# Optimization experiments

Measured on AMD Instinct MI355X. Metric: run time of the kernel, lower is better.

The kernel has to match this reference:

```python
import jax, jax.numpy as jnp
import numpy as np

SLEN, BSZ = 256, 8
NUM_HEAD, DIM_HEAD = 16, 64
IN_DIM = NUM_HEAD * DIM_HEAD  # 1024
LN_EPS = 1e-5


def setup_inputs() -> dict:
    key = jax.random.key(0)
    ks = jax.random.split(key, 6)
    std = 1.0 / np.sqrt(DIM_HEAD)
    std_q = 0.01 / np.sqrt(DIM_HEAD)
    beta_init = -1.0
    h = jax.random.normal(ks[0], (SLEN, BSZ, IN_DIM), dtype=jnp.float32)
    W_y = std * jax.random.normal(ks[1], (1, NUM_HEAD, DIM_HEAD, DIM_HEAD), dtype=jnp.float32)
    W_q = std_q * jax.random.normal(ks[2], (1, NUM_HEAD, DIM_HEAD, DIM_HEAD), dtype=jnp.float32)
    W_k = std * jax.random.normal(ks[3], (1, NUM_HEAD, DIM_HEAD, DIM_HEAD), dtype=jnp.float32)
    w_b = beta_init + std * jax.random.normal(ks[4], (1, NUM_HEAD, DIM_HEAD, 4), dtype=jnp.float32)
    out_w = std * jax.random.normal(ks[5], (IN_DIM, NUM_HEAD * DIM_HEAD), dtype=jnp.float32)
    ln_gamma = jnp.ones((IN_DIM,), dtype=jnp.float32)
    ln_beta = jnp.zeros((IN_DIM,), dtype=jnp.float32)
    return {"h": h, "W_y": W_y, "W_q": W_q, "W_k": W_k, "w_b": w_b,
            "out_w": out_w, "ln_gamma": ln_gamma, "ln_beta": ln_beta}


def _srwm_scan(x, W_y, W_q, W_k, w_b):
    # x: (slen, B, H, d); fast weights broadcast over batch
    bsz = x.shape[1]
    Wy0 = jnp.broadcast_to(W_y, (bsz,) + W_y.shape[1:])
    Wq0 = jnp.broadcast_to(W_q, (bsz,) + W_q.shape[1:])
    Wk0 = jnp.broadcast_to(W_k, (bsz,) + W_k.shape[1:])
    wb0 = jnp.broadcast_to(w_b, (bsz,) + w_b.shape[1:])

    def step(carry, x_t):
        Wy, Wq, Wk, wb = carry
        # generate outputs with W_{t-1}
        y = jnp.einsum('bhij,bhj->bhi', Wy, x_t)
        q = jax.nn.softmax(jnp.einsum('bhij,bhj->bhi', Wq, x_t), axis=-1)
        k = jax.nn.softmax(jnp.einsum('bhij,bhj->bhi', Wk, x_t), axis=-1)
        beta = jax.nn.sigmoid(jnp.einsum('bhjc,bhj->bhc', wb, x_t))  # (B,H,4)
        qmk = q - k
        def upd(W, b):
            dv = jnp.einsum('bhij,bhj->bhi', W, qmk)  # W q - W k
            return W + b[..., None, None] * dv[..., :, None] * k[..., None, :]
        Wy_n = upd(Wy, beta[..., 0])
        Wq_n = upd(Wq, beta[..., 1])
        Wk_n = upd(Wk, beta[..., 2])
        dvb = jnp.einsum('bhjc,bhj->bhc', wb, qmk)  # (B,H,4)
        wb_n = wb + beta[..., 3][..., None, None] * k[..., :, None] * dvb[..., None, :]
        return (Wy_n, Wq_n, Wk_n, wb_n), y

    _, ys = jax.lax.scan(step, (Wy0, Wq0, Wk0, wb0), x)
    return ys  # (slen, B, H, d)


def reference(h, W_y, W_q, W_k, w_b, out_w, ln_gamma, ln_beta):
    slen, bsz, _ = h.shape
    x = h.reshape(slen, bsz, NUM_HEAD, DIM_HEAD)
    ys = _srwm_scan(x, W_y, W_q, W_k, w_b)
    out = ys.reshape(slen, bsz, NUM_HEAD * DIM_HEAD)
    out = out @ out_w.T  # (slen, bsz, in_dim), no bias
    # dropout p=0 (eval): identity
    mu = jnp.mean(h, axis=-1, keepdims=True)
    var = jnp.mean(jnp.square(h - mu), axis=-1, keepdims=True)
    h_ln = (h - mu) * jax.lax.rsqrt(var + LN_EPS) * ln_gamma + ln_beta
    return h_ln + out
```

## Files before the change

### kernel.cpp

```cpp
#include <hip/hip_runtime.h>
#include <hip/hip_bf16.h>

#define SLEN  256
#define BSZ   8
#define NHEAD 16
#define DHEAD 64
#define INDIM 1024
#define LN_EPS 1e-5f

typedef __attribute__((ext_vector_type(4))) float f32x4;
typedef __attribute__((ext_vector_type(8))) short bf16x8;

__device__ __forceinline__ int f_as_i(float f) { union { float f; int i; } u; u.f = f; return u.i; }
__device__ __forceinline__ float i_as_f(int i) { union { float f; int i; } u; u.i = i; return u.f; }

__device__ inline unsigned short f2bf(float x) {
  __hip_bfloat16 b = __float2bfloat16(x);
  union { __hip_bfloat16 b; unsigned short u; } cv;
  cv.b = b;
  return cv.u;
}

template <int CTRL>
__device__ __forceinline__ float dpp0(float x) {
  return i_as_f(__builtin_amdgcn_update_dpp(0, f_as_i(x), CTRL, 0xF, 0xF, true));
}

__device__ __forceinline__ float pair_other(float x) { return dpp0<0xB1>(x); }

__device__ __forceinline__ float wave_sum64(float v) {
  v += dpp0<0x111>(v);
  v += dpp0<0x112>(v);
  v += dpp0<0x114>(v);
  v += dpp0<0x118>(v);
  v += dpp0<0x142>(v);
  v += dpp0<0x143>(v);
  return i_as_f(__builtin_amdgcn_readlane(f_as_i(v), 63));
}

__global__ __launch_bounds__(512, 1) void scan_prep_k(
    const float* __restrict__ h,
    const float* __restrict__ Wy0,
    const float* __restrict__ Wq0,
    const float* __restrict__ Wk0,
    const float* __restrict__ wb0,
    const float* __restrict__ outw,
    unsigned short* __restrict__ outw_bf,
    float* __restrict__ stats,
    unsigned short* __restrict__ ys_bf) {
  const int bid = blockIdx.x;
  const int tid = threadIdx.x;

  if (bid >= 128) {
    const int pb = bid - 128;
    if (pb < 512) {
      int i = (pb * 512 + tid) * 4;
      float4 v = *(const float4*)(outw + i);
      ushort4 o;
      o.x = f2bf(v.x); o.y = f2bf(v.y); o.z = f2bf(v.z); o.w = f2bf(v.w);
      *(ushort4*)(outw_bf + i) = o;
    } else {
      int r = pb - 512;
      const float* row = h + (size_t)r * INDIM;
      float2 v = *(const float2*)(row + tid * 2);
      float s  = v.x + v.y;
      float s2 = v.x * v.x + v.y * v.y;
      s  = wave_sum64(s);
      s2 = wave_sum64(s2);
      __shared__ float ls[8], ls2[8];
      int wvv = tid >> 6;
      if ((tid & 63) == 0) { ls[wvv] = s; ls2[wvv] = s2; }
      __syncthreads();
      if (tid == 0) {
        float S = 0.f, S2 = 0.f;
        #pragma unroll
        for (int i = 0; i < 8; ++i) { S += ls[i]; S2 += ls2[i]; }
        float mu = S * (1.0f / INDIM);
        float var = S2 * (1.0f / INDIM) - mu * mu;
        stats[2 * r]     = mu;
        stats[2 * r + 1] = rsqrtf(var + LN_EPS);
      }
    }
    return;
  }

  const int chain = bid;
  const int b    = chain >> 4;
  const int head = chain & 15;
  const int wv   = __builtin_amdgcn_readfirstlane(tid >> 6);
  const int lane = tid & 63;

  __shared__ __align__(16) float xbuf[2][64];
  __shared__ __align__(16) float eqk[2][2][64];
  __shared__ __align__(16) float ssub[2][4];
  __shared__ __align__(16) float betabuf[2][4];

  const float* xrow0 = h + (size_t)b * INDIM + head * DHEAD;

  if (wv < 6) {
    const int m    = wv >> 1;
    const int half = wv & 1;
    const int r    = half * 32 + (lane >> 1);
    const int j0   = (lane & 1) * 32;
    const float* Wsel = (m == 0) ? Wy0 : ((m == 1) ? Wq0 : Wk0);
    const float* wrow = Wsel + (size_t)head * DHEAD * DHEAD + (size_t)r * DHEAD + j0;
    float w[32];
    #pragma unroll
    for (int g = 0; g < 8; ++g) {
      float4 t4 = *(const float4*)(wrow + g * 4);
      w[g * 4] = t4.x; w[g * 4 + 1] = t4.y; w[g * 4 + 2] = t4.z; w[g * 4 + 3] = t4.w;
    }
    __syncthreads();

    for (int t = 0; t < SLEN; ++t) {
      const int buf = t & 1;
      float a0 = 0.f, a1 = 0.f, a2 = 0.f, a3 = 0.f;
      #pragma unroll
      for (int g = 0; g < 8; ++g) {
        float4 x4 = *(const float4*)(&xbuf[buf][j0 + g * 4]);
        a0 += w[g * 4]     * x4.x;
        a1 += w[g * 4 + 1] * x4.y;
        a2 += w[g * 4 + 2] * x4.z;
        a3 += w[g * 4 + 3] * x4.w;
      }
      float v = (a0 + a1) + (a2 + a3);
      v += pair_other(v);

      if (m == 0) {
        if (!(lane & 1))
          ys_bf[(size_t)(t * BSZ + b) * INDIM + head * DHEAD + r] = f2bf(v);
      } else {
        float e = __expf(v);
        if (!(lane & 1)) eqk[buf][m - 1][r] = e;
        float sh = wave_sum64(e) * 0.5f;
        if (lane == 0) ssub[buf][(m - 1) * 2 + half] = sh;
      }
      __syncthreads();

      float4 ss = *(const float4*)(&ssub[buf][0]);
      float rq = __fdividef(1.f, ss.x + ss.y);
      float rk = __fdividef(1.f, ss.z + ss.w);
      float bet = betabuf[buf][m];
      float ek[32];
      float dq0 = 0.f, dq1 = 0.f, dq2 = 0.f, dq3 = 0.f;
      float dk0 = 0.f, dk1 = 0.f, dk2 = 0.f, dk3 = 0.f;
      #pragma unroll
      for (int g = 0; g < 8; ++g) {
        float4 q4 = *(const float4*)(&eqk[buf][0][j0 + g * 4]);
        float4 k4 = *(const float4*)(&eqk[buf][1][j0 + g * 4]);
        ek[g * 4] = k4.x; ek[g * 4 + 1] = k4.y; ek[g * 4 + 2] = k4.z; ek[g * 4 + 3] = k4.w;
        dq0 += w[g * 4]     * q4.x;
        dq1 += w[g * 4 + 1] * q4.y;
        dq2 += w[g * 4 + 2] * q4.z;
        dq3 += w[g * 4 + 3] * q4.w;
        dk0 += w[g * 4]     * k4.x;
        dk1 += w[g * 4 + 1] * k4.y;
        dk2 += w[g * 4 + 2] * k4.z;
        dk3 += w[g * 4 + 3] * k4.w;
      }
      float dv = rq * ((dq0 + dq1) + (dq2 + dq3)) - rk * ((dk0 + dk1) + (dk2 + dk3));
      dv += pair_other(dv);
      float c = bet * dv * rk;
      #pragma unroll
      for (int g = 0; g < 8; ++g) {
        w[g * 4]     += c * ek[g * 4];
        w[g * 4 + 1] += c * ek[g * 4 + 1];
        w[g * 4 + 2] += c * ek[g * 4 + 2];
        w[g * 4 + 3] += c * ek[g * 4 + 3];
      }
    }
  } else if (wv == 6) {
    const float* wbrow = wb0 + (size_t)head * DHEAD * 4 + lane * 4;
    float4 wbv = *(const float4*)wbrow;
    __syncthreads();

    for (int t = 0; t < SLEN; ++t) {
      const int buf = t & 1;
      float xv = xbuf[buf][lane];
      float p0 = wave_sum64(wbv.x * xv);
      float p1 = wave_sum64(wbv.y * xv);
      float p2 = wave_sum64(wbv.z * xv);
      float p3 = wave_sum64(wbv.w * xv);
      float b0 = __fdividef(1.f, 1.f + __expf(-p0));
      float b1 = __fdividef(1.f, 1.f + __expf(-p1));
      float b2 = __fdividef(1.f, 1.f + __expf(-p2));
      float b3 = __fdividef(1.f, 1.f + __expf(-p3));
      if (lane == 0) {
        *(float4*)(&betabuf[buf][0]) = (float4){b0, b1, b2, b3};
      }
      __syncthreads();

      float4 ss = *(const float4*)(&ssub[buf][0]);
      float rq = __fdividef(1.f, ss.x + ss.y);
      float rk = __fdividef(1.f, ss.z + ss.w);
      float qv = rq * eqk[buf][0][lane];
      float kv = rk * eqk[buf][1][lane];
      float qmk = qv - kv;
      float g0 = wave_sum64(wbv.x * qmk);
      float g1 = wave_sum64(wbv.y * qmk);
      float g2 = wave_sum64(wbv.z * qmk);
      float g3 = wave_sum64(wbv.w * qmk);
      float cl = b3 * kv;
      wbv.x += cl * g0; wbv.y += cl * g1; wbv.z += cl * g2; wbv.w += cl * g3;
    }
  } else {
    float x0 = xrow0[lane];
    xbuf[0][lane] = x0;
    float xn1 = xrow0[(size_t)1 * BSZ * INDIM + lane];
    __syncthreads();

    for (int t = 0; t < SLEN; ++t) {
      if (t + 1 < SLEN) xbuf[(t + 1) & 1][lane] = xn1;
      float xn2 = 0.f;
      if (t + 2 < SLEN) xn2 = xrow0[(size_t)(t + 2) * BSZ * INDIM + lane];
      __syncthreads();
      xn1 = xn2;
    }
  }
}

__global__ __launch_bounds__(256, 1) void gemm_ln_k(
    const unsigned short* __restrict__ A,
    const unsigned short* __restrict__ B,
    const float* __restrict__ h,
    const float* __restrict__ stats,
    const float* __restrict__ gamma,
    const float* __restrict__ lbeta,
    float* __restrict__ out) {
  const int bx = blockIdx.x & 15;
  const int by = blockIdx.x >> 4;
  const int tid = threadIdx.x;
  const int wave = tid >> 6, lane = tid & 63;
  const int wr = wave >> 1, wc = wave & 1;
  const int rbase = by * 32 + wr * 16;
  const int nbase = bx * 64 + wc * 32;
  const int l16 = lane & 15;
  const int kofs = (lane >> 4) * 8;

  const short* Ap = (const short*)A;
  const short* Bp = (const short*)B;

  f32x4 acc[2];
  acc[0] = (f32x4){0.f, 0.f, 0.f, 0.f};
  acc[1] = (f32x4){0.f, 0.f, 0.f, 0.f};

  const short* arow = Ap + (size_t)(rbase + l16) * INDIM + kofs;
  const short* brow[2];
  #pragma unroll
  for (int j = 0; j < 2; ++j)
    brow[j] = Bp + (size_t)(nbase + j * 16 + l16) * INDIM + kofs;

  bf16x8 Ab[4], Bb[4][2];
  Ab[0] = *(const bf16x8*)(arow);
  Ab[1] = *(const bf16x8*)(arow + 32);
  #pragma unroll
  for (int j = 0; j < 2; ++j) {
    Bb[0][j] = *(const bf16x8*)(brow[j]);
    Bb[1][j] = *(const bf16x8*)(brow[j] + 32);
  }

  for (int n8 = 0; n8 < 8; ++n8) {
    #pragma unroll
    for (int c = 0; c < 4; ++c) {
      const int n = n8 * 4 + c;
      if (n + 2 < 32) {
        const int kk = (n + 2) * 32;
        const int pb = (c + 2) & 3;
        Ab[pb] = *(const bf16x8*)(arow + kk);
        #pragma unroll
        for (int j = 0; j < 2; ++j)
          Bb[pb][j] = *(const bf16x8*)(brow[j] + kk);
      }
      #pragma unroll
      for (int j = 0; j < 2; ++j)
        acc[j] = __builtin_amdgcn_mfma_f32_16x16x32_bf16(Ab[c & 3], Bb[c & 3][j], acc[j], 0, 0, 0);
    }
  }

  const int rq4 = (lane >> 4) * 4;
  #pragma unroll
  for (int reg = 0; reg < 4; ++reg) {
    int r = rbase + rq4 + reg;
    float mu = stats[2 * r], rs = stats[2 * r + 1];
    #pragma unroll
    for (int j = 0; j < 2; ++j) {
      int n = nbase + j * 16 + l16;
      float hv = h[(size_t)r * INDIM + n];
      float hln = (hv - mu) * rs * gamma[n] + lbeta[n];
      out[(size_t)r * INDIM + n] = acc[j][reg] + hln;
    }
  }
}

extern "C" void kernel_launch(void* const* d_in, const int* in_sizes, int n_in,
                              void* d_out, int out_size, void* d_ws, size_t ws_size,
                              hipStream_t stream) {
  const float* h    = (const float*)d_in[0];
  const float* Wy   = (const float*)d_in[1];
  const float* Wq   = (const float*)d_in[2];
  const float* Wk   = (const float*)d_in[3];
  const float* wb   = (const float*)d_in[4];
  const float* outw = (const float*)d_in[5];
  const float* gam  = (const float*)d_in[6];
  const float* bet  = (const float*)d_in[7];
  float* out = (float*)d_out;

  char* ws = (char*)d_ws;
  unsigned short* ys_bf   = (unsigned short*)ws;
  unsigned short* outw_bf = (unsigned short*)(ws + (size_t)2048 * 1024 * 2);
  float* stats            = (float*)(ws + (size_t)2048 * 1024 * 2 + (size_t)1024 * 1024 * 2);

  scan_prep_k<<<128 + 512 + 2048, 512, 0, stream>>>(h, Wy, Wq, Wk, wb, outw,
                                                    outw_bf, stats, ys_bf);
  gemm_ln_k<<<1024, 256, 0, stream>>>(ys_bf, outw_bf, h, stats, gam, bet, out);
}
```

Measured before the change: 357.1 us.

## Skew scan recurrence, fuse LayerNorm into prep, retile GEMM to accumulate

The scan loop is reordered so each step first applies the previous update and then computes the next output in one phase. This removes one barrier per timestep. x is prefetched into registers through a triple buffer, and the beta wave is skewed to match. The LayerNorm output is now written directly in the prep kernel, so the GEMM tile doubles to 64 rows, gains a block swizzle, and does a read-modify-write add into out. Occupancy hints become 2 blocks per CU. The costs are more register pressure and an extra read of out in the GEMM.

```diff
diff --git a/kernel.cpp b/kernel.cpp
--- a/kernel.cpp
+++ b/kernel.cpp
@@ -25,7 +25,6 @@
 __device__ __forceinline__ float dpp0(float x) {
   return i_as_f(__builtin_amdgcn_update_dpp(0, f_as_i(x), CTRL, 0xF, 0xF, true));
 }
-
 __device__ __forceinline__ float pair_other(float x) { return dpp0<0xB1>(x); }
 
 __device__ __forceinline__ float wave_sum64(float v) {
@@ -38,15 +37,17 @@
   return i_as_f(__builtin_amdgcn_readlane(f_as_i(v), 63));
 }
 
-__global__ __launch_bounds__(512, 1) void scan_prep_k(
+__global__ __launch_bounds__(512, 2) void scan_prep_k(
     const float* __restrict__ h,
     const float* __restrict__ Wy0,
     const float* __restrict__ Wq0,
     const float* __restrict__ Wk0,
     const float* __restrict__ wb0,
     const float* __restrict__ outw,
+    const float* __restrict__ gamma,
+    const float* __restrict__ lbeta,
     unsigned short* __restrict__ outw_bf,
-    float* __restrict__ stats,
+    float* __restrict__ outp,
     unsigned short* __restrict__ ys_bf) {
   const int bid = blockIdx.x;
   const int tid = threadIdx.x;
@@ -67,7 +68,7 @@
       float s2 = v.x * v.x + v.y * v.y;
       s  = wave_sum64(s);
       s2 = wave_sum64(s2);
-      __shared__ float ls[8], ls2[8];
+      __shared__ float ls[8], ls2[8], sstat[2];
       int wvv = tid >> 6;
       if ((tid & 63) == 0) { ls[wvv] = s; ls2[wvv] = s2; }
       __syncthreads();
@@ -77,9 +78,17 @@
         for (int i = 0; i < 8; ++i) { S += ls[i]; S2 += ls2[i]; }
         float mu = S * (1.0f / INDIM);
         float var = S2 * (1.0f / INDIM) - mu * mu;
-        stats[2 * r]     = mu;
-        stats[2 * r + 1] = rsqrtf(var + LN_EPS);
-      }
+        sstat[0] = mu;
+        sstat[1] = rsqrtf(var + LN_EPS);
+      }
+      __syncthreads();
+      float mu = sstat[0], rs = sstat[1];
+      float2 g2 = *(const float2*)(gamma + tid * 2);
+      float2 b2 = *(const float2*)(lbeta + tid * 2);
+      float2 o;
+      o.x = (v.x - mu) * rs * g2.x + b2.x;
+      o.y = (v.y - mu) * rs * g2.y + b2.y;
+      *(float2*)(outp + (size_t)r * INDIM + tid * 2) = o;
     }
     return;
   }
@@ -90,12 +99,76 @@
   const int wv   = __builtin_amdgcn_readfirstlane(tid >> 6);
   const int lane = tid & 63;
 
-  __shared__ __align__(16) float xbuf[2][64];
+  __shared__ __align__(16) float xbuf[3][64];
   __shared__ __align__(16) float eqk[2][2][64];
   __shared__ __align__(16) float ssub[2][4];
   __shared__ __align__(16) float betabuf[2][4];
 
   const float* xrow0 = h + (size_t)b * INDIM + head * DHEAD;
+
+#define PUBLISH(T, V) {                                                          \
+    if (m == 0) {                                                                \
+      if (!(lane & 1))                                                           \
+        ys_bf[(size_t)((T) * BSZ + b) * INDIM + head * DHEAD + r] = f2bf(V);     \
+    } else {                                                                     \
+      float e_ = __expf(V);                                                      \
+      if (!(lane & 1)) eqk[(T) & 1][m - 1][r] = e_;                              \
+      float sh_ = wave_sum64(e_) * 0.5f;                                         \
+      if (lane == 0) ssub[(T) & 1][(m - 1) * 2 + half] = sh_;                    \
+    }                                                                            \
+  }
+
+#define PHASE(T, XC, XN) {                                                       \
+    const int bp_ = ((T) - 1) & 1;                                               \
+    float4 ss4 = *(const float4*)(&ssub[bp_][0]);                                \
+    float4 bb4 = *(const float4*)(&betabuf[bp_][0]);                             \
+    float4 q4[8], k4[8];                                                         \
+    _Pragma("unroll")                                                            \
+    for (int g = 0; g < 8; ++g) {                                                \
+      q4[g] = *(const float4*)(&eqk[bp_][0][j0 + g * 4]);                        \
+      k4[g] = *(const float4*)(&eqk[bp_][1][j0 + g * 4]);                        \
+    }                                                                            \
+    if ((T) + 1 < SLEN) {                                                        \
+      const float* xsrc_ = &xbuf[((T) + 1) % 3][j0];                             \
+      _Pragma("unroll")                                                          \
+      for (int g = 0; g < 8; ++g) {                                              \
+        float4 x4_ = *(const float4*)(xsrc_ + g * 4);                            \
+        XN[g * 4] = x4_.x; XN[g * 4 + 1] = x4_.y;                                \
+        XN[g * 4 + 2] = x4_.z; XN[g * 4 + 3] = x4_.w;                            \
+      }                                                                          \
+    }                                                                            \
+    float dq0 = 0.f, dq1 = 0.f, dq2 = 0.f, dq3 = 0.f;                            \
+    float dk0 = 0.f, dk1 = 0.f, dk2 = 0.f, dk3 = 0.f;                            \
+    _Pragma("unroll")                                                            \
+    for (int g = 0; g < 8; ++g) {                                                \
+      dq0 += w[g * 4]     * q4[g].x; dq1 += w[g * 4 + 1] * q4[g].y;              \
+      dq2 += w[g * 4 + 2] * q4[g].z; dq3 += w[g * 4 + 3] * q4[g].w;              \
+      dk0 += w[g * 4]     * k4[g].x; dk1 += w[g * 4 + 1] * k4[g].y;              \
+      dk2 += w[g * 4 + 2] * k4[g].z; dk3 += w[g * 4 + 3] * k4[g].w;              \
+    }                                                                            \
+    float rq = __fdividef(1.f, ss4.x + ss4.y);                                   \
+    float rk = __fdividef(1.f, ss4.z + ss4.w);                                   \
+    float dv = rq * ((dq0 + dq1) + (dq2 + dq3))                                  \
+             - rk * ((dk0 + dk1) + (dk2 + dk3));                                 \
+    dv += pair_other(dv);                                                        \
+    float bet_ = (m == 0) ? bb4.x : ((m == 1) ? bb4.y : bb4.z);                  \
+    float c_ = bet_ * dv * rk;                                                   \
+    _Pragma("unroll")                                                            \
+    for (int g = 0; g < 8; ++g) {                                                \
+      w[g * 4]     += c_ * k4[g].x; w[g * 4 + 1] += c_ * k4[g].y;                \
+      w[g * 4 + 2] += c_ * k4[g].z; w[g * 4 + 3] += c_ * k4[g].w;                \
+    }                                                                            \
+    float a0 = 0.f, a1 = 0.f, a2 = 0.f, a3 = 0.f;                                \
+    _Pragma("unroll")                                                            \
+    for (int g = 0; g < 8; ++g) {                                                \
+      a0 += w[g * 4]     * XC[g * 4];     a1 += w[g * 4 + 1] * XC[g * 4 + 1];    \
+      a2 += w[g * 4 + 2] * XC[g * 4 + 2]; a3 += w[g * 4 + 3] * XC[g * 4 + 3];    \
+    }                                                                            \
+    float v_ = (a0 + a1) + (a2 + a3);                                            \
+    v_ += pair_other(v_);                                                        \
+    PUBLISH(T, v_);                                                              \
+    __syncthreads();                                                             \
+  }
 
   if (wv < 6) {
     const int m    = wv >> 1;
@@ -110,73 +183,45 @@
       float4 t4 = *(const float4*)(wrow + g * 4);
       w[g * 4] = t4.x; w[g * 4 + 1] = t4.y; w[g * 4 + 2] = t4.z; w[g * 4 + 3] = t4.w;
     }
+    float xA[32], xB[32];
+    #pragma unroll
+    for (int g = 0; g < 8; ++g) {
+      float4 t4 = *(const float4*)(xrow0 + j0 + g * 4);
+      xA[g * 4] = t4.x; xA[g * 4 + 1] = t4.y; xA[g * 4 + 2] = t4.z; xA[g * 4 + 3] = t4.w;
+    }
     __syncthreads();
 
-    for (int t = 0; t < SLEN; ++t) {
-      const int buf = t & 1;
+    {
       float a0 = 0.f, a1 = 0.f, a2 = 0.f, a3 = 0.f;
       #pragma unroll
       for (int g = 0; g < 8; ++g) {
-        float4 x4 = *(const float4*)(&xbuf[buf][j0 + g * 4]);
-        a0 += w[g * 4]     * x4.x;
-        a1 += w[g * 4 + 1] * x4.y;
-        a2 += w[g * 4 + 2] * x4.z;
-        a3 += w[g * 4 + 3] * x4.w;
-      }
-      float v = (a0 + a1) + (a2 + a3);
-      v += pair_other(v);
-
-      if (m == 0) {
-        if (!(lane & 1))
-          ys_bf[(size_t)(t * BSZ + b) * INDIM + head * DHEAD + r] = f2bf(v);
-      } else {
-        float e = __expf(v);
-        if (!(lane & 1)) eqk[buf][m - 1][r] = e;
-        float sh = wave_sum64(e) * 0.5f;
-        if (lane == 0) ssub[buf][(m - 1) * 2 + half] = sh;
-      }
-      __syncthreads();
-
-      float4 ss = *(const float4*)(&ssub[buf][0]);
-      float rq = __fdividef(1.f, ss.x + ss.y);
-      float rk = __fdividef(1.f, ss.z + ss.w);
-      float bet = betabuf[buf][m];
-      float ek[32];
-      float dq0 = 0.f, dq1 = 0.f, dq2 = 0.f, dq3 = 0.f;
-      float dk0 = 0.f, dk1 = 0.f, dk2 = 0.f, dk3 = 0.f;
+        a0 += w[g * 4]     * xA[g * 4];     a1 += w[g * 4 + 1] * xA[g * 4 + 1];
+        a2 += w[g * 4 + 2] * xA[g * 4 + 2]; a3 += w[g * 4 + 3] * xA[g * 4 + 3];
+      }
+      float v0 = (a0 + a1) + (a2 + a3);
+      v0 += pair_other(v0);
+      PUBLISH(0, v0);
       #pragma unroll
       for (int g = 0; g < 8; ++g) {
-        float4 q4 = *(const float4*)(&eqk[buf][0][j0 + g * 4]);
-        float4 k4 = *(const float4*)(&eqk[buf][1][j0 + g * 4]);
-        ek[g * 4] = k4.x; ek[g * 4 + 1] = k4.y; ek[g * 4 + 2] = k4.z; ek[g * 4 + 3] = k4.w;
-        dq0 += w[g * 4]     * q4.x;
-        dq1 += w[g * 4 + 1] * q4.y;
-        dq2 += w[g * 4 + 2] * q4.z;
-        dq3 += w[g * 4 + 3] * q4.w;
-        dk0 += w[g * 4]     * k4.x;
-        dk1 += w[g * 4 + 1] * k4.y;
-        dk2 += w[g * 4 + 2] * k4.z;
-        dk3 += w[g * 4 + 3] * k4.w;
-      }
-      float dv = rq * ((dq0 + dq1) + (dq2 + dq3)) - rk * ((dk0 + dk1) + (dk2 + dk3));
-      dv += pair_other(dv);
-      float c = bet * dv * rk;
-      #pragma unroll
-      for (int g = 0; g < 8; ++g) {
-        w[g * 4]     += c * ek[g * 4];
-        w[g * 4 + 1] += c * ek[g * 4 + 1];
-        w[g * 4 + 2] += c * ek[g * 4 + 2];
-        w[g * 4 + 3] += c * ek[g * 4 + 3];
-      }
-    }
+        float4 x4 = *(const float4*)(&xbuf[1][j0 + g * 4]);
+        xB[g * 4] = x4.x; xB[g * 4 + 1] = x4.y; xB[g * 4 + 2] = x4.z; xB[g * 4 + 3] = x4.w;
+      }
+      __syncthreads();
+    }
+    for (int tt = 1; tt <= 253; tt += 2) {
+      PHASE(tt, xB, xA);
+      PHASE(tt + 1, xA, xB);
+    }
+    PHASE(255, xB, xA);
   } else if (wv == 6) {
     const float* wbrow = wb0 + (size_t)head * DHEAD * 4 + lane * 4;
     float4 wbv = *(const float4*)wbrow;
+    float xv = xrow0[lane];
+    float xn = xrow0[(size_t)BSZ * INDIM + lane];
+    float b3prev = 0.f;
     __syncthreads();
 
-    for (int t = 0; t < SLEN; ++t) {
-      const int buf = t & 1;
-      float xv = xbuf[buf][lane];
+    {
       float p0 = wave_sum64(wbv.x * xv);
       float p1 = wave_sum64(wbv.y * xv);
       float p2 = wave_sum64(wbv.z * xv);
@@ -185,54 +230,69 @@
       float b1 = __fdividef(1.f, 1.f + __expf(-p1));
       float b2 = __fdividef(1.f, 1.f + __expf(-p2));
       float b3 = __fdividef(1.f, 1.f + __expf(-p3));
-      if (lane == 0) {
-        *(float4*)(&betabuf[buf][0]) = (float4){b0, b1, b2, b3};
-      }
-      __syncthreads();
-
-      float4 ss = *(const float4*)(&ssub[buf][0]);
-      float rq = __fdividef(1.f, ss.x + ss.y);
-      float rk = __fdividef(1.f, ss.z + ss.w);
-      float qv = rq * eqk[buf][0][lane];
-      float kv = rk * eqk[buf][1][lane];
+      if (lane == 0) *(float4*)(&betabuf[0][0]) = (float4){b0, b1, b2, b3};
+      b3prev = b3;
+      xv = xn;
+      xn = xrow0[(size_t)2 * BSZ * INDIM + lane];
+      __syncthreads();
+    }
+    for (int t = 1; t < SLEN; ++t) {
+      const int bp = (t - 1) & 1;
+      float4 ss4 = *(const float4*)(&ssub[bp][0]);
+      float eq = eqk[bp][0][lane];
+      float ek = eqk[bp][1][lane];
+      float rq = __fdividef(1.f, ss4.x + ss4.y);
+      float rk = __fdividef(1.f, ss4.z + ss4.w);
+      float qv = rq * eq, kv = rk * ek;
       float qmk = qv - kv;
       float g0 = wave_sum64(wbv.x * qmk);
       float g1 = wave_sum64(wbv.y * qmk);
       float g2 = wave_sum64(wbv.z * qmk);
       float g3 = wave_sum64(wbv.w * qmk);
-      float cl = b3 * kv;
+      float cl = b3prev * kv;
       wbv.x += cl * g0; wbv.y += cl * g1; wbv.z += cl * g2; wbv.w += cl * g3;
+      float p0 = wave_sum64(wbv.x * xv);
+      float p1 = wave_sum64(wbv.y * xv);
+      float p2 = wave_sum64(wbv.z * xv);
+      float p3 = wave_sum64(wbv.w * xv);
+      float b0 = __fdividef(1.f, 1.f + __expf(-p0));
+      float b1 = __fdividef(1.f, 1.f + __expf(-p1));
+      float b2 = __fdividef(1.f, 1.f + __expf(-p2));
+      float b3 = __fdividef(1.f, 1.f + __expf(-p3));
+      if (lane == 0) *(float4*)(&betabuf[t & 1][0]) = (float4){b0, b1, b2, b3};
+      b3prev = b3;
+      xv = xn;
+      if (t + 2 < SLEN) xn = xrow0[(size_t)(t + 2) * BSZ * INDIM + lane];
+      __syncthreads();
     }
   } else {
-    float x0 = xrow0[lane];
-    xbuf[0][lane] = x0;
-    float xn1 = xrow0[(size_t)1 * BSZ * INDIM + lane];
+    xbuf[1][lane] = xrow0[(size_t)BSZ * INDIM + lane];
+    xbuf[2][lane] = xrow0[(size_t)2 * BSZ * INDIM + lane];
+    float g1 = xrow0[(size_t)3 * BSZ * INDIM + lane];
     __syncthreads();
 
     for (int t = 0; t < SLEN; ++t) {
-      if (t + 1 < SLEN) xbuf[(t + 1) & 1][lane] = xn1;
-      float xn2 = 0.f;
-      if (t + 2 < SLEN) xn2 = xrow0[(size_t)(t + 2) * BSZ * INDIM + lane];
-      __syncthreads();
-      xn1 = xn2;
-    }
-  }
-}
-
-__global__ __launch_bounds__(256, 1) void gemm_ln_k(
+      if (t + 3 < SLEN) xbuf[t % 3][lane] = g1;
+      if (t + 4 < SLEN) g1 = xrow0[(size_t)(t + 4) * BSZ * INDIM + lane];
+      __syncthreads();
+    }
+  }
+#undef PHASE
+#undef PUBLISH
+}
+
+__global__ __launch_bounds__(256, 2) void gemm_acc_k(
     const unsigned short* __restrict__ A,
     const unsigned short* __restrict__ B,
-    const float* __restrict__ h,
-    const float* __restrict__ stats,
-    const float* __restrict__ gamma,
-    const float* __restrict__ lbeta,
     float* __restrict__ out) {
-  const int bx = blockIdx.x & 15;
-  const int by = blockIdx.x >> 4;
+  const int bid0 = blockIdx.x;
+  const int swz = (bid0 & 7) * 64 + (bid0 >> 3);
+  const int bx = swz & 15;
+  const int by = swz >> 4;
   const int tid = threadIdx.x;
   const int wave = tid >> 6, lane = tid & 63;
   const int wr = wave >> 1, wc = wave & 1;
-  const int rbase = by * 32 + wr * 16;
+  const int rbase = by * 64 + wr * 32;
   const int nbase = bx * 64 + wc * 32;
   const int l16 = lane & 15;
   const int kofs = (lane >> 4) * 8;
@@ -240,54 +300,60 @@
   const short* Ap = (const short*)A;
   const short* Bp = (const short*)B;
 
-  f32x4 acc[2];
-  acc[0] = (f32x4){0.f, 0.f, 0.f, 0.f};
-  acc[1] = (f32x4){0.f, 0.f, 0.f, 0.f};
-
-  const short* arow = Ap + (size_t)(rbase + l16) * INDIM + kofs;
+  f32x4 acc[2][2];
+  #pragma unroll
+  for (int i = 0; i < 2; ++i)
+    #pragma unroll
+    for (int j = 0; j < 2; ++j)
+      acc[i][j] = (f32x4){0.f, 0.f, 0.f, 0.f};
+
+  const short* arow[2];
   const short* brow[2];
+  #pragma unroll
+  for (int i = 0; i < 2; ++i)
+    arow[i] = Ap + (size_t)(rbase + i * 16 + l16) * INDIM + kofs;
   #pragma unroll
   for (int j = 0; j < 2; ++j)
     brow[j] = Bp + (size_t)(nbase + j * 16 + l16) * INDIM + kofs;
 
-  bf16x8 Ab[4], Bb[4][2];
-  Ab[0] = *(const bf16x8*)(arow);
-  Ab[1] = *(const bf16x8*)(arow + 32);
-  #pragma unroll
-  for (int j = 0; j < 2; ++j) {
-    Bb[0][j] = *(const bf16x8*)(brow[j]);
-    Bb[1][j] = *(const bf16x8*)(brow[j] + 32);
-  }
-
-  for (int n8 = 0; n8 < 8; ++n8) {
-    #pragma unroll
-    for (int c = 0; c < 4; ++c) {
-      const int n = n8 * 4 + c;
-      if (n + 2 < 32) {
-        const int kk = (n + 2) * 32;
-        const int pb = (c + 2) & 3;
-        Ab[pb] = *(const bf16x8*)(arow + kk);
-        #pragma unroll
-        for (int j = 0; j < 2; ++j)
-          Bb[pb][j] = *(const bf16x8*)(brow[j] + kk);
-      }
+  bf16x8 Ab[4][2], Bb[4][2];
+  #pragma unroll
+  for (int c = 0; c < 3; ++c)
+    #pragma unroll
+    for (int i = 0; i < 2; ++i) {
+      Ab[c][i] = *(const bf16x8*)(arow[i] + c * 32);
+      Bb[c][i] = *(const bf16x8*)(brow[i] + c * 32);
+    }
+
+  #pragma unroll
+  for (int c = 0; c < 32; ++c) {
+    if (c + 3 < 32) {
+      const int pb = (c + 3) & 3;
+      #pragma unroll
+      for (int i = 0; i < 2; ++i) {
+        Ab[pb][i] = *(const bf16x8*)(arow[i] + (c + 3) * 32);
+        Bb[pb][i] = *(const bf16x8*)(brow[i] + (c + 3) * 32);
+      }
+    }
+    #pragma unroll
+    for (int i = 0; i < 2; ++i)
       #pragma unroll
       for (int j = 0; j < 2; ++j)
-        acc[j] = __builtin_amdgcn_mfma_f32_16x16x32_bf16(Ab[c & 3], Bb[c & 3][j], acc[j], 0, 0, 0);
-    }
+        acc[i][j] = __builtin_amdgcn_mfma_f32_16x16x32_bf16(Ab[c & 3][i], Bb[c & 3][j], acc[i][j], 0, 0, 0);
   }
 
   const int rq4 = (lane >> 4) * 4;
   #pragma unroll
-  for (int reg = 0; reg < 4; ++reg) {
-    int r = rbase + rq4 + reg;
-    float mu = stats[2 * r], rs = stats[2 * r + 1];
-    #pragma unroll
-    for (int j = 0; j < 2; ++j) {
-      int n = nbase + j * 16 + l16;
-      float hv = h[(size_t)r * INDIM + n];
-      float hln = (hv - mu) * rs * gamma[n] + lbeta[n];
-      out[(size_t)r * INDIM + n] = acc[j][reg] + hln;
+  for (int i = 0; i < 2; ++i) {
+    #pragma unroll
+    for (int reg = 0; reg < 4; ++reg) {
+      int r = rbase + i * 16 + rq4 + reg;
+      #pragma unroll
+      for (int j = 0; j < 2; ++j) {
+        int n = nbase + j * 16 + l16;
+        size_t idx = (size_t)r * INDIM + n;
+        out[idx] += acc[i][j][reg];
+      }
     }
   }
 }
@@ -308,9 +374,8 @@
   char* ws = (char*)d_ws;
   unsigned short* ys_bf   = (unsigned short*)ws;
   unsigned short* outw_bf = (unsigned short*)(ws + (size_t)2048 * 1024 * 2);
-  float* stats            = (float*)(ws + (size_t)2048 * 1024 * 2 + (size_t)1024 * 1024 * 2);
 
   scan_prep_k<<<128 + 512 + 2048, 512, 0, stream>>>(h, Wy, Wq, Wk, wb, outw,
-                                                    outw_bf, stats, ys_bf);
-  gemm_ln_k<<<1024, 256, 0, stream>>>(ys_bf, outw_bf, h, stats, gam, bet, out);
-}
+                                                    gam, bet, outw_bf, out, ys_bf);
+  gemm_acc_k<<<512, 256, 0, stream>>>(ys_bf, outw_bf, out);
+}
```

After: 347.9 us. 1.03x faster.

## Restructure scan step ordering, pack q/k as bf16, LDS-tiled GEMM accumulating into LN output

Applied to the files above, without the earlier changes.

The scan now defers each step's fast-weight update to the start of the next step. Each wave loads its own x directly from global memory instead of going through a feeder wave, and q/k exponentials are packed as bf16 pairs in one shared buffer, which cuts LDS traffic. LayerNorm output is written in the prep kernel, and the GEMM is rewritten with LDS double-buffered 64x64 tiles, block swizzling and a read-modify-write accumulate into out. Packing q/k to bf16 lowers precision of the update path, and the extra read of out in the GEMM epilogue adds memory traffic.

```diff
diff --git a/kernel.cpp b/kernel.cpp
--- a/kernel.cpp
+++ b/kernel.cpp
@@ -25,7 +25,6 @@
 __device__ __forceinline__ float dpp0(float x) {
   return i_as_f(__builtin_amdgcn_update_dpp(0, f_as_i(x), CTRL, 0xF, 0xF, true));
 }
-
 __device__ __forceinline__ float pair_other(float x) { return dpp0<0xB1>(x); }
 
 __device__ __forceinline__ float wave_sum64(float v) {
@@ -45,8 +44,10 @@
     const float* __restrict__ Wk0,
     const float* __restrict__ wb0,
     const float* __restrict__ outw,
+    const float* __restrict__ gamma,
+    const float* __restrict__ lbeta,
     unsigned short* __restrict__ outw_bf,
-    float* __restrict__ stats,
+    float* __restrict__ outp,
     unsigned short* __restrict__ ys_bf) {
   const int bid = blockIdx.x;
   const int tid = threadIdx.x;
@@ -67,19 +68,27 @@
       float s2 = v.x * v.x + v.y * v.y;
       s  = wave_sum64(s);
       s2 = wave_sum64(s2);
-      __shared__ float ls[8], ls2[8];
+      __shared__ float ls[8], ls2[8], sstat[2];
       int wvv = tid >> 6;
       if ((tid & 63) == 0) { ls[wvv] = s; ls2[wvv] = s2; }
       __syncthreads();
       if (tid == 0) {
         float S = 0.f, S2 = 0.f;
         #pragma unroll
-        for (int i = 0; i < 8; ++i) { S += ls[i]; S2 += ls2[i]; }
+        for (int i2 = 0; i2 < 8; ++i2) { S += ls[i2]; S2 += ls2[i2]; }
         float mu = S * (1.0f / INDIM);
         float var = S2 * (1.0f / INDIM) - mu * mu;
-        stats[2 * r]     = mu;
-        stats[2 * r + 1] = rsqrtf(var + LN_EPS);
-      }
+        sstat[0] = mu;
+        sstat[1] = rsqrtf(var + LN_EPS);
+      }
+      __syncthreads();
+      float mu = sstat[0], rs = sstat[1];
+      float2 g2 = *(const float2*)(gamma + tid * 2);
+      float2 b2 = *(const float2*)(lbeta + tid * 2);
+      float2 o;
+      o.x = (v.x - mu) * rs * g2.x + b2.x;
+      o.y = (v.y - mu) * rs * g2.y + b2.y;
+      *(float2*)(outp + (size_t)r * INDIM + tid * 2) = o;
     }
     return;
   }
@@ -90,12 +99,8 @@
   const int wv   = __builtin_amdgcn_readfirstlane(tid >> 6);
   const int lane = tid & 63;
 
-  __shared__ __align__(16) float xbuf[2][64];
-  __shared__ __align__(16) float eqk[2][2][64];
-  __shared__ __align__(16) float ssub[2][4];
-  __shared__ __align__(16) float betabuf[2][4];
-
-  const float* xrow0 = h + (size_t)b * INDIM + head * DHEAD;
+  __shared__ __align__(16) unsigned int qkp[2][64];
+  __shared__ __align__(16) float meta[2][8];
 
   if (wv < 6) {
     const int m    = wv >> 1;
@@ -104,24 +109,63 @@
     const int j0   = (lane & 1) * 32;
     const float* Wsel = (m == 0) ? Wy0 : ((m == 1) ? Wq0 : Wk0);
     const float* wrow = Wsel + (size_t)head * DHEAD * DHEAD + (size_t)r * DHEAD + j0;
-    float w[32];
+    float wt[32];
     #pragma unroll
     for (int g = 0; g < 8; ++g) {
       float4 t4 = *(const float4*)(wrow + g * 4);
-      w[g * 4] = t4.x; w[g * 4 + 1] = t4.y; w[g * 4 + 2] = t4.z; w[g * 4 + 3] = t4.w;
-    }
-    __syncthreads();
+      wt[g * 4] = t4.x; wt[g * 4 + 1] = t4.y; wt[g * 4 + 2] = t4.z; wt[g * 4 + 3] = t4.w;
+    }
+    const float* xg0 = h + (size_t)b * INDIM + head * DHEAD + j0;
 
     for (int t = 0; t < SLEN; ++t) {
-      const int buf = t & 1;
+      const int buf = t & 1, bp = buf ^ 1;
+      float4 xf[8];
+      {
+        const float* xg = xg0 + (size_t)t * (BSZ * INDIM);
+        #pragma unroll
+        for (int g = 0; g < 8; ++g) xf[g] = *(const float4*)(xg + g * 4);
+      }
+      if (t > 0) {
+        float4 ssb = *(const float4*)(&meta[bp][0]);
+        float4 btb = *(const float4*)(&meta[bp][4]);
+        uint4 kp[8];
+        float dq0 = 0.f, dq1 = 0.f, dq2 = 0.f, dq3 = 0.f;
+        float dk0 = 0.f, dk1 = 0.f, dk2 = 0.f, dk3 = 0.f;
+        #pragma unroll
+        for (int g = 0; g < 8; ++g) {
+          uint4 p = *(const uint4*)(&qkp[bp][j0 + g * 4]);
+          kp[g] = p;
+          dq0 += wt[g * 4]     * i_as_f((int)(p.x << 16));
+          dk0 += wt[g * 4]     * i_as_f((int)(p.x & 0xFFFF0000u));
+          dq1 += wt[g * 4 + 1] * i_as_f((int)(p.y << 16));
+          dk1 += wt[g * 4 + 1] * i_as_f((int)(p.y & 0xFFFF0000u));
+          dq2 += wt[g * 4 + 2] * i_as_f((int)(p.z << 16));
+          dk2 += wt[g * 4 + 2] * i_as_f((int)(p.z & 0xFFFF0000u));
+          dq3 += wt[g * 4 + 3] * i_as_f((int)(p.w << 16));
+          dk3 += wt[g * 4 + 3] * i_as_f((int)(p.w & 0xFFFF0000u));
+        }
+        float rq = __fdividef(1.f, ssb.x + ssb.y);
+        float rk = __fdividef(1.f, ssb.z + ssb.w);
+        float dv = rq * ((dq0 + dq1) + (dq2 + dq3)) - rk * ((dk0 + dk1) + (dk2 + dk3));
+        dv += pair_other(dv);
+        float bet = (m == 0) ? btb.x : ((m == 1) ? btb.y : btb.z);
+        float c = bet * dv * rk;
+        #pragma unroll
+        for (int g = 0; g < 8; ++g) {
+          uint4 p = kp[g];
+          wt[g * 4]     += c * i_as_f((int)(p.x & 0xFFFF0000u));
+          wt[g * 4 + 1] += c * i_as_f((int)(p.y & 0xFFFF0000u));
+          wt[g * 4 + 2] += c * i_as_f((int)(p.z & 0xFFFF0000u));
+          wt[g * 4 + 3] += c * i_as_f((int)(p.w & 0xFFFF0000u));
+        }
+      }
       float a0 = 0.f, a1 = 0.f, a2 = 0.f, a3 = 0.f;
       #pragma unroll
       for (int g = 0; g < 8; ++g) {
-        float4 x4 = *(const float4*)(&xbuf[buf][j0 + g * 4]);
-        a0 += w[g * 4]     * x4.x;
-        a1 += w[g * 4 + 1] * x4.y;
-        a2 += w[g * 4 + 2] * x4.z;
-        a3 += w[g * 4 + 3] * x4.w;
+        a0 += wt[g * 4]     * xf[g].x;
+        a1 += wt[g * 4 + 1] * xf[g].y;
+        a2 += wt[g * 4 + 2] * xf[g].z;
+        a3 += wt[g * 4 + 3] * xf[g].w;
       }
       float v = (a0 + a1) + (a2 + a3);
       v += pair_other(v);
@@ -131,52 +175,39 @@
           ys_bf[(size_t)(t * BSZ + b) * INDIM + head * DHEAD + r] = f2bf(v);
       } else {
         float e = __expf(v);
-        if (!(lane & 1)) eqk[buf][m - 1][r] = e;
-        float sh = wave_sum64(e) * 0.5f;
-        if (lane == 0) ssub[buf][(m - 1) * 2 + half] = sh;
+        unsigned int eu = ((unsigned int)f_as_i(e)) & 0xFFFF0000u;
+        if (!(lane & 1))
+          ((unsigned short*)&qkp[buf][r])[m - 1] = (unsigned short)(eu >> 16);
+        float sh = wave_sum64(i_as_f((int)eu)) * 0.5f;
+        if (lane == 0) meta[buf][(m - 1) * 2 + half] = sh;
       }
       __syncthreads();
-
-      float4 ss = *(const float4*)(&ssub[buf][0]);
-      float rq = __fdividef(1.f, ss.x + ss.y);
-      float rk = __fdividef(1.f, ss.z + ss.w);
-      float bet = betabuf[buf][m];
-      float ek[32];
-      float dq0 = 0.f, dq1 = 0.f, dq2 = 0.f, dq3 = 0.f;
-      float dk0 = 0.f, dk1 = 0.f, dk2 = 0.f, dk3 = 0.f;
-      #pragma unroll
-      for (int g = 0; g < 8; ++g) {
-        float4 q4 = *(const float4*)(&eqk[buf][0][j0 + g * 4]);
-        float4 k4 = *(const float4*)(&eqk[buf][1][j0 + g * 4]);
-        ek[g * 4] = k4.x; ek[g * 4 + 1] = k4.y; ek[g * 4 + 2] = k4.z; ek[g * 4 + 3] = k4.w;
-        dq0 += w[g * 4]     * q4.x;
-        dq1 += w[g * 4 + 1] * q4.y;
-        dq2 += w[g * 4 + 2] * q4.z;
-        dq3 += w[g * 4 + 3] * q4.w;
-        dk0 += w[g * 4]     * k4.x;
-        dk1 += w[g * 4 + 1] * k4.y;
-        dk2 += w[g * 4 + 2] * k4.z;
-        dk3 += w[g * 4 + 3] * k4.w;
-      }
-      float dv = rq * ((dq0 + dq1) + (dq2 + dq3)) - rk * ((dk0 + dk1) + (dk2 + dk3));
-      dv += pair_other(dv);
-      float c = bet * dv * rk;
-      #pragma unroll
-      for (int g = 0; g < 8; ++g) {
-        w[g * 4]     += c * ek[g * 4];
-        w[g * 4 + 1] += c * ek[g * 4 + 1];
-        w[g * 4 + 2] += c * ek[g * 4 + 2];
-        w[g * 4 + 3] += c * ek[g * 4 + 3];
-      }
     }
   } else if (wv == 6) {
     const float* wbrow = wb0 + (size_t)head * DHEAD * 4 + lane * 4;
     float4 wbv = *(const float4*)wbrow;
-    __syncthreads();
+    const float* xl = h + (size_t)b * INDIM + head * DHEAD + lane;
+    float xv = xl[0];
+    float xn = xl[(size_t)BSZ * INDIM];
+    float b3prev = 0.f;
 
     for (int t = 0; t < SLEN; ++t) {
-      const int buf = t & 1;
-      float xv = xbuf[buf][lane];
+      const int buf = t & 1, bp = buf ^ 1;
+      if (t > 0) {
+        unsigned int d = qkp[bp][lane];
+        float4 ssb = *(const float4*)(&meta[bp][0]);
+        float rq = __fdividef(1.f, ssb.x + ssb.y);
+        float rk = __fdividef(1.f, ssb.z + ssb.w);
+        float qv = rq * i_as_f((int)(d << 16));
+        float kv = rk * i_as_f((int)(d & 0xFFFF0000u));
+        float qmk = qv - kv;
+        float g0 = wave_sum64(wbv.x * qmk);
+        float g1 = wave_sum64(wbv.y * qmk);
+        float g2 = wave_sum64(wbv.z * qmk);
+        float g3 = wave_sum64(wbv.w * qmk);
+        float cl = b3prev * kv;
+        wbv.x += cl * g0; wbv.y += cl * g1; wbv.z += cl * g2; wbv.w += cl * g3;
+      }
       float p0 = wave_sum64(wbv.x * xv);
       float p1 = wave_sum64(wbv.y * xv);
       float p2 = wave_sum64(wbv.z * xv);
@@ -185,109 +216,100 @@
       float b1 = __fdividef(1.f, 1.f + __expf(-p1));
       float b2 = __fdividef(1.f, 1.f + __expf(-p2));
       float b3 = __fdividef(1.f, 1.f + __expf(-p3));
-      if (lane == 0) {
-        *(float4*)(&betabuf[buf][0]) = (float4){b0, b1, b2, b3};
-      }
+      if (lane == 0) *(float4*)(&meta[buf][4]) = (float4){b0, b1, b2, b3};
+      b3prev = b3;
+      xv = xn;
+      if (t + 2 < SLEN) xn = xl[(size_t)(t + 2) * BSZ * INDIM];
       __syncthreads();
-
-      float4 ss = *(const float4*)(&ssub[buf][0]);
-      float rq = __fdividef(1.f, ss.x + ss.y);
-      float rk = __fdividef(1.f, ss.z + ss.w);
-      float qv = rq * eqk[buf][0][lane];
-      float kv = rk * eqk[buf][1][lane];
-      float qmk = qv - kv;
-      float g0 = wave_sum64(wbv.x * qmk);
-      float g1 = wave_sum64(wbv.y * qmk);
-      float g2 = wave_sum64(wbv.z * qmk);
-      float g3 = wave_sum64(wbv.w * qmk);
-      float cl = b3 * kv;
-      wbv.x += cl * g0; wbv.y += cl * g1; wbv.z += cl * g2; wbv.w += cl * g3;
     }
   } else {
-    float x0 = xrow0[lane];
-    xbuf[0][lane] = x0;
-    float xn1 = xrow0[(size_t)1 * BSZ * INDIM + lane];
-    __syncthreads();
-
-    for (int t = 0; t < SLEN; ++t) {
-      if (t + 1 < SLEN) xbuf[(t + 1) & 1][lane] = xn1;
-      float xn2 = 0.f;
-      if (t + 2 < SLEN) xn2 = xrow0[(size_t)(t + 2) * BSZ * INDIM + lane];
-      __syncthreads();
-      xn1 = xn2;
-    }
-  }
-}
-
-__global__ __launch_bounds__(256, 1) void gemm_ln_k(
+    for (int t = 0; t < SLEN; ++t) __syncthreads();
+  }
+}
+
+#define LDA 40
+__global__ __launch_bounds__(256, 2) void gemm_acc_k(
     const unsigned short* __restrict__ A,
     const unsigned short* __restrict__ B,
-    const float* __restrict__ h,
-    const float* __restrict__ stats,
-    const float* __restrict__ gamma,
-    const float* __restrict__ lbeta,
     float* __restrict__ out) {
-  const int bx = blockIdx.x & 15;
-  const int by = blockIdx.x >> 4;
+  __shared__ __align__(16) unsigned short Al[2][64 * LDA];
+  __shared__ __align__(16) unsigned short Bl[2][64 * LDA];
+
+  const int bid0 = blockIdx.x;
+  const int swz = (bid0 & 7) * 64 + (bid0 >> 3);
+  const int bx = swz & 15;
+  const int by = swz >> 4;
   const int tid = threadIdx.x;
   const int wave = tid >> 6, lane = tid & 63;
   const int wr = wave >> 1, wc = wave & 1;
-  const int rbase = by * 32 + wr * 16;
-  const int nbase = bx * 64 + wc * 32;
   const int l16 = lane & 15;
   const int kofs = (lane >> 4) * 8;
 
   const short* Ap = (const short*)A;
   const short* Bp = (const short*)B;
 
-  f32x4 acc[2];
-  acc[0] = (f32x4){0.f, 0.f, 0.f, 0.f};
-  acc[1] = (f32x4){0.f, 0.f, 0.f, 0.f};
-
-  const short* arow = Ap + (size_t)(rbase + l16) * INDIM + kofs;
-  const short* brow[2];
+  const int srow = tid >> 2;
+  const int scol = (tid & 3) * 8;
+  const short* ags = Ap + (size_t)(by * 64 + srow) * INDIM + scol;
+  const short* bgs = Bp + (size_t)(bx * 64 + srow) * INDIM + scol;
+  unsigned short* adst = &Al[0][srow * LDA + scol];
+  unsigned short* bdst = &Bl[0][srow * LDA + scol];
+
+  f32x4 acc[2][2];
   #pragma unroll
-  for (int j = 0; j < 2; ++j)
-    brow[j] = Bp + (size_t)(nbase + j * 16 + l16) * INDIM + kofs;
-
-  bf16x8 Ab[4], Bb[4][2];
-  Ab[0] = *(const bf16x8*)(arow);
-  Ab[1] = *(const bf16x8*)(arow + 32);
-  #pragma unroll
-  for (int j = 0; j < 2; ++j) {
-    Bb[0][j] = *(const bf16x8*)(brow[j]);
-    Bb[1][j] = *(const bf16x8*)(brow[j] + 32);
-  }
-
-  for (int n8 = 0; n8 < 8; ++n8) {
-    #pragma unroll
-    for (int c = 0; c < 4; ++c) {
-      const int n = n8 * 4 + c;
-      if (n + 2 < 32) {
-        const int kk = (n + 2) * 32;
-        const int pb = (c + 2) & 3;
-        Ab[pb] = *(const bf16x8*)(arow + kk);
-        #pragma unroll
-        for (int j = 0; j < 2; ++j)
-          Bb[pb][j] = *(const bf16x8*)(brow[j] + kk);
-      }
+  for (int i = 0; i < 2; ++i)
+    #pragma unroll
+    for (int j = 0; j < 2; ++j)
+      acc[i][j] = (f32x4){0.f, 0.f, 0.f, 0.f};
+
+  {
+    uint4 ga = *(const uint4*)(ags);
+    uint4 gb = *(const uint4*)(bgs);
+    *(uint4*)(adst) = ga;
+    *(uint4*)(bdst) = gb;
+  }
+  __syncthreads();
+
+  int buf = 0;
+  for (int it = 0; it < 32; ++it) {
+    uint4 ga, gb;
+    const bool more = (it + 1 < 32);
+    if (more) {
+      ga = *(const uint4*)(ags + (it + 1) * 32);
+      gb = *(const uint4*)(bgs + (it + 1) * 32);
+    }
+    bf16x8 af[2], bfv[2];
+    #pragma unroll
+    for (int i = 0; i < 2; ++i)
+      af[i] = *(const bf16x8*)(&Al[buf][(wr * 32 + i * 16 + l16) * LDA + kofs]);
+    #pragma unroll
+    for (int j = 0; j < 2; ++j)
+      bfv[j] = *(const bf16x8*)(&Bl[buf][(wc * 32 + j * 16 + l16) * LDA + kofs]);
+    #pragma unroll
+    for (int i = 0; i < 2; ++i)
       #pragma unroll
       for (int j = 0; j < 2; ++j)
-        acc[j] = __builtin_amdgcn_mfma_f32_16x16x32_bf16(Ab[c & 3], Bb[c & 3][j], acc[j], 0, 0, 0);
-    }
+        acc[i][j] = __builtin_amdgcn_mfma_f32_16x16x32_bf16(af[i], bfv[j], acc[i][j], 0, 0, 0);
+    if (more) {
+      *(uint4*)(adst + (buf ^ 1) * 64 * LDA) = ga;
+      *(uint4*)(bdst + (buf ^ 1) * 64 * LDA) = gb;
+    }
+    __syncthreads();
+    buf ^= 1;
   }
 
   const int rq4 = (lane >> 4) * 4;
   #pragma unroll
-  for (int reg = 0; reg < 4; ++reg) {
-    int r = rbase + rq4 + reg;
-    float mu = stats[2 * r], rs = stats[2 * r + 1];
-    #pragma unroll
-    for (int j = 0; j < 2; ++j) {
-      int n = nbase + j * 16 + l16;
-      float hv = h[(size_t)r * INDIM + n];
-      float hln = (hv - mu) * rs * gamma[n] + lbeta[n];
-      out[(size_t)r * INDIM + n] = acc[j][reg] + hln;
+  for (int i = 0; i < 2; ++i) {
+    #pragma unroll
+    for (int reg = 0; reg < 4; ++reg) {
+      int r = by * 64 + wr * 32 + i * 16 + rq4 + reg;
+      #pragma unroll
+      for (int j = 0; j < 2; ++j) {
+        int n = bx * 64 + wc * 32 + j * 16 + l16;
+        size_t idx = (size_t)r * INDIM + n;
+        out[idx] += acc[i][j][reg];
+      }
     }
   }
 }
@@ -308,9 +330,8 @@
   char* ws = (char*)d_ws;
   unsigned short* ys_bf   = (unsigned short*)ws;
   unsigned short* outw_bf = (unsigned short*)(ws + (size_t)2048 * 1024 * 2);
-  float* stats            = (float*)(ws + (size_t)2048 * 1024 * 2 + (size_t)1024 * 1024 * 2);
 
   scan_prep_k<<<128 + 512 + 2048, 512, 0, stream>>>(h, Wy, Wq, Wk, wb, outw,
-                                                    outw_bf, stats, ys_bf);
-  gemm_ln_k<<<1024, 256, 0, stream>>>(ys_bf, outw_bf, h, stats, gam, bet, out);
-}
+                                                    gam, bet, outw_bf, out, ys_bf);
+  gemm_acc_k<<<512, 256, 0, stream>>>(ys_bf, outw_bf, out);
+}
```

Result: slower. 401.2 us (+12.4%).
